# Kernel tuning notes

Hardware: AMD Instinct MI355X
Metric: run time of the kernel (lower is better)

## Reference

```python
import jax, jax.numpy as jnp
import numpy as np

B, T, V, S = 64, 512, 1296, 32
BLANK = 0
NEG = jnp.float32(-1e30)  # log-space -inf surrogate (keeps grads finite)


def setup_inputs() -> dict:
    key = jax.random.key(0)
    k1, k2 = jax.random.split(key)
    logits = jax.random.normal(k1, (B, T, V), dtype=jnp.float32)
    # CTC targets must not contain the blank index (0)
    targets = jax.random.randint(k2, (B, S), 1, V).astype(jnp.int64)
    input_lengths = jnp.full((B,), T, dtype=jnp.int32)
    target_lengths = jnp.full((B,), S, dtype=jnp.int32)
    return {"logits": logits, "targets": targets,
            "input_lengths": input_lengths, "target_lengths": target_lengths}


def _ctc_loss(log_probs, targets, input_lengths, target_lengths):
    """CTC negative log-likelihood, reduction='mean' (per-sample / target_len, then batch mean)."""
    Bb, Tt, Vv = log_probs.shape
    Ss = targets.shape[1]
    L = 2 * Ss + 1  # extended label sequence: blank-interleaved

    ext = jnp.full((Bb, L), BLANK, dtype=targets.dtype).at[:, 1::2].set(targets)  # (B,L)
    # log-prob of each extended label at each time: (B,T,L)
    lp_ext = jnp.take_along_axis(log_probs, jnp.broadcast_to(ext[:, None, :], (Bb, Tt, L)), axis=2)

    # transition s-2 -> s allowed iff ext[s] is non-blank (s odd) and ext[s] != ext[s-2]
    pos = jnp.arange(L)
    ext_m2 = jnp.pad(ext, ((0, 0), (2, 0)), constant_values=-1)[:, :L]
    skip_ok = (pos[None, :] % 2 == 1) & (ext != ext_m2)  # (B,L)

    alpha0 = (jnp.full((Bb, L), NEG)
              .at[:, 0].set(lp_ext[:, 0, 0])
              .at[:, 1].set(lp_ext[:, 0, 1]))

    def step(alpha, lp_t):
        a1 = alpha
        a2 = jnp.pad(alpha[:, :-1], ((0, 0), (1, 0)), constant_values=NEG)
        a3 = jnp.where(skip_ok, jnp.pad(alpha[:, :-2], ((0, 0), (2, 0)), constant_values=NEG), NEG)
        new = jnp.logaddexp(jnp.logaddexp(a1, a2), a3) + lp_t
        return new, new

    _, alphas_rest = jax.lax.scan(step, alpha0, jnp.swapaxes(lp_ext, 0, 1)[1:])  # (T-1,B,L)
    alphas = jnp.concatenate([alpha0[None], alphas_rest], axis=0)  # (T,B,L)

    bi = jnp.arange(Bb)
    alpha_last = alphas[input_lengths - 1, bi]  # (B,L)
    l_end = alpha_last[bi, 2 * target_lengths]       # final blank
    l_lab = alpha_last[bi, 2 * target_lengths - 1]   # final label
    nll = -jnp.logaddexp(l_end, l_lab)               # (B,)
    nll = jnp.where(jnp.isinf(nll) | (nll > 1e29), 0.0, nll)  # zero_infinity=True
    return jnp.mean(nll / target_lengths.astype(nll.dtype))    # reduction='mean'


def reference(logits, targets, input_lengths, target_lengths):
    log_probs = jax.nn.log_softmax(logits, axis=-1)
    return _ctc_loss(log_probs, targets, input_lengths, target_lengths)
```

## Files before the change

kernel.cpp:

```cpp
#include <hip/hip_runtime.h>
#include <math.h>

#define BB 64
#define TT 512
#define VV 1296
#define SS 32
#define NST 64
#define NG  (TT/4)
#define NEGV (-1e30f)
#define LOG2E 1.44269504088896340736f
#define LN2   0.69314718055994530942f

#define EXP2(x) __builtin_amdgcn_exp2f(x)
#define LOG2(x) __builtin_amdgcn_logf(x)

__device__ __forceinline__ float dpp_shr1(float old, float src) {
    return __int_as_float(__builtin_amdgcn_update_dpp(
        __float_as_int(old), __float_as_int(src), 0x138, 0xf, 0xf, false));
}
__device__ __forceinline__ float dpp_shl1(float old, float src) {
    return __int_as_float(__builtin_amdgcn_update_dpp(
        __float_as_int(old), __float_as_int(src), 0x130, 0xf, 0xf, false));
}

__global__ __launch_bounds__(256) void k_lse_gather(
    const float* __restrict__ logits,
    const int* __restrict__ targets,
    float* __restrict__ lp_ext,
    float* __restrict__ out)
{
    const int wid  = threadIdx.x >> 6;
    const int lane = threadIdx.x & 63;
    const int bt   = blockIdx.x * 4 + wid;
    const int b    = bt >> 9;
    const int t    = bt & (TT - 1);

    if (bt == 0 && lane == 0) out[0] = 0.f;

    const float* row = logits + (size_t)bt * VV;
    const float4* row4 = (const float4*)row;

    float4 v[5];
    #pragma unroll
    for (int k = 0; k < 5; ++k) v[k] = row4[lane + 64 * k];
    float4 vx = row4[320 + (lane & 3)];
    if (lane >= 4) { vx.x = NEGV; vx.y = NEGV; vx.z = NEGV; vx.w = NEGV; }

    float s = 0.f;
    #pragma unroll
    for (int k = 0; k < 5; ++k)
        s += __expf(v[k].x) + __expf(v[k].y) + __expf(v[k].z) + __expf(v[k].w);
    s += __expf(vx.x) + __expf(vx.y) + __expf(vx.z) + __expf(vx.w);
    #pragma unroll
    for (int off = 1; off < 64; off <<= 1) s += __shfl_xor(s, off, 64);

    const float norm = __logf(s);

    const int lab = (lane & 1) ? 0 : targets[b * SS + (lane >> 1)];
    const float lp2 = (row[lab] - norm) * LOG2E;
    lp_ext[(((size_t)b * NG + (t >> 2)) * NST + lane) * 4 + (t & 3)] = lp2;
}

#define PFV 6

__global__ __launch_bounds__(64) void k_alpha(
    const float* __restrict__ lp_ext,
    const int* __restrict__ targets,
    const int* __restrict__ in_len,
    const int* __restrict__ tgt_len,
    float* __restrict__ out)
{
    const int b    = blockIdx.x;
    const int lane = threadIdx.x;
    const float4* lpv = (const float4*)(lp_ext + (size_t)b * NG * NST * 4);
    const int Ti = in_len[b];
    const int Sb = tgt_len[b];

    bool skip = false;
    if (!(lane & 1) && lane >= 2) {
        const int j = lane >> 1;
        skip = (targets[b * SS + j] != targets[b * SS + j - 1]);
    }

    const float4 g0 = lpv[lane];

    float alpha = (lane == 0) ? g0.x : NEGV;
    float c0    = __shfl(g0.x, 1, 64);

#define STEP(LPS)                                                            \
    {                                                                        \
        const float lps_ = (LPS);                                            \
           \
        const float lpbk_ = (lane & 1) ? lps_ : dpp_shl1(lps_, lps_);        \
        const float a1_ = alpha;                                             \
        const float a2_ = dpp_shr1(c0, alpha);         \
        float a3_       = dpp_shr1(NEGV, a2_);               \
        a3_ = skip ? a3_ : NEGV;          \
        c0 += lpbk_;                                     \
        const float mx_ = fmaxf(fmaxf(a1_, a2_), a3_);           \
        const float ml_ = mx_ + lps_;                 \
        alpha = LOG2(EXP2(a1_ - mx_) + EXP2(a2_ - mx_) +                     \
                     EXP2(a3_ - mx_)) + ml_;                                 \
    }

    if (Ti > 1) STEP(g0.y);
    if (Ti > 2) STEP(g0.z);
    if (Ti > 3) STEP(g0.w);

    float4 bufv[PFV];
    #pragma unroll
    for (int i = 0; i < PFV; ++i) {
        int gg = 1 + i; if (gg > NG - 1) gg = NG - 1;
        bufv[i] = lpv[gg * NST + lane];
    }

    int g = 1;
    while (g + PFV <= NG) {
        #pragma unroll
        for (int i = 0; i < PFV; ++i) {
            const float4 cur = bufv[i];
            int gp = g + i + PFV; if (gp > NG - 1) gp = NG - 1;
            bufv[i] = lpv[(size_t)gp * NST + lane];
            const int t0 = (g + i) * 4;
            if (t0 + 3 < Ti) {
                STEP(cur.x); STEP(cur.y); STEP(cur.z); STEP(cur.w);
            } else {
                if (t0 + 0 < Ti) STEP(cur.x);
                if (t0 + 1 < Ti) STEP(cur.y);
                if (t0 + 2 < Ti) STEP(cur.z);
                if (t0 + 3 < Ti) STEP(cur.w);
            }
        }
        g += PFV;
    }
    #pragma unroll
    for (int i = 0; i < PFV; ++i) {
        const int gi = g + i;
        if (gi <= NG - 1) {
            const float4 cur = bufv[i];
            const int t0 = gi * 4;
            if (t0 + 3 < Ti) {
                STEP(cur.x); STEP(cur.y); STEP(cur.z); STEP(cur.w);
            } else {
                if (t0 + 0 < Ti) STEP(cur.x);
                if (t0 + 1 < Ti) STEP(cur.y);
                if (t0 + 2 < Ti) STEP(cur.z);
                if (t0 + 3 < Ti) STEP(cur.w);
            }
        }
    }
#undef STEP

    const float vll = __shfl(alpha, 2 * Sb - 2, 64);
    const float vle = __shfl(alpha, 2 * Sb - 1, 64);

    if (lane == 0) {
        const float mx = fmaxf(vle, vll);
        float nll = -LN2 * (mx + LOG2(EXP2(vle - mx) + EXP2(vll - mx)));
        if (isinf(nll) || nll > 1e29f) nll = 0.f;
        atomicAdd(out, nll / ((float)Sb * (float)BB));
    }
}

extern "C" void kernel_launch(void* const* d_in, const int* in_sizes, int n_in,
                              void* d_out, int out_size, void* d_ws, size_t ws_size,
                              hipStream_t stream) {
    const float* logits   = (const float*)d_in[0];
    const int*   targets  = (const int*)d_in[1];
    const int*   in_len   = (const int*)d_in[2];
    const int*   tgt_len  = (const int*)d_in[3];
    float*       out      = (float*)d_out;

    float* lp_ext = (float*)d_ws;

    k_lse_gather<<<BB * TT / 4, 256, 0, stream>>>(logits, targets, lp_ext, out);
    k_alpha<<<BB, 64, 0, stream>>>(lp_ext, targets, in_len, tgt_len, out);
}
```

Before: 270.7 us.

## Fuse log-softmax gather and alpha recursion via last-block-per-batch counter

Merges the two kernels into one launch. Each block computes log-softmax and gathers for 4 timesteps, then an atomic counter per batch lets the last finishing block run the sequential alpha recursion using coherent atomic loads. A second counter lets the final batch reduce the per-sample NLLs without a float atomicAdd. This removes a kernel launch boundary and lets alpha recursions for early-finishing batches overlap with remaining gather work. In exchange it adds a memset, atomic traffic and uncached coherent loads.

```diff
diff --git a/kernel.cpp b/kernel.cpp
--- a/kernel.cpp
+++ b/kernel.cpp
@@ -14,6 +14,8 @@
 #define EXP2(x) __builtin_amdgcn_exp2f(x)
 #define LOG2(x) __builtin_amdgcn_logf(x)
 
+#define PFV 6
+
 __device__ __forceinline__ float dpp_shr1(float old, float src) {
     return __int_as_float(__builtin_amdgcn_update_dpp(
         __float_as_int(old), __float_as_int(src), 0x138, 0xf, 0xf, false));
@@ -23,55 +25,74 @@
         __float_as_int(old), __float_as_int(src), 0x130, 0xf, 0xf, false));
 }
 
-__global__ __launch_bounds__(256) void k_lse_gather(
+__device__ __forceinline__ float4 load_f4_coherent(const float4* p) {
+    unsigned long long* q = (unsigned long long*)p;
+    unsigned long long lo = __hip_atomic_load(q,     __ATOMIC_RELAXED, __HIP_MEMORY_SCOPE_AGENT);
+    unsigned long long hi = __hip_atomic_load(q + 1, __ATOMIC_RELAXED, __HIP_MEMORY_SCOPE_AGENT);
+    float4 r;
+    r.x = __uint_as_float((unsigned int)lo);
+    r.y = __uint_as_float((unsigned int)(lo >> 32));
+    r.z = __uint_as_float((unsigned int)hi);
+    r.w = __uint_as_float((unsigned int)(hi >> 32));
+    return r;
+}
+
+__global__ __launch_bounds__(256) void k_ctc_fused(
     const float* __restrict__ logits,
     const int* __restrict__ targets,
+    const int* __restrict__ in_len,
+    const int* __restrict__ tgt_len,
+    unsigned int* __restrict__ cnt,
+    unsigned int* __restrict__ dcnt,
+    float* __restrict__ nlls,
     float* __restrict__ lp_ext,
     float* __restrict__ out)
 {
     const int wid  = threadIdx.x >> 6;
     const int lane = threadIdx.x & 63;
-    const int bt   = blockIdx.x * 4 + wid;
-    const int b    = bt >> 9;
-    const int t    = bt & (TT - 1);
-
-    if (bt == 0 && lane == 0) out[0] = 0.f;
-
-    const float* row = logits + (size_t)bt * VV;
-    const float4* row4 = (const float4*)row;
-
-    float4 v[5];
-    #pragma unroll
-    for (int k = 0; k < 5; ++k) v[k] = row4[lane + 64 * k];
-    float4 vx = row4[320 + (lane & 3)];
-    if (lane >= 4) { vx.x = NEGV; vx.y = NEGV; vx.z = NEGV; vx.w = NEGV; }
-
-    float s = 0.f;
-    #pragma unroll
-    for (int k = 0; k < 5; ++k)
-        s += __expf(v[k].x) + __expf(v[k].y) + __expf(v[k].z) + __expf(v[k].w);
-    s += __expf(vx.x) + __expf(vx.y) + __expf(vx.z) + __expf(vx.w);
-    #pragma unroll
-    for (int off = 1; off < 64; off <<= 1) s += __shfl_xor(s, off, 64);
-
-    const float norm = __logf(s);
-
-    const int lab = (lane & 1) ? 0 : targets[b * SS + (lane >> 1)];
-    const float lp2 = (row[lab] - norm) * LOG2E;
-    lp_ext[(((size_t)b * NG + (t >> 2)) * NST + lane) * 4 + (t & 3)] = lp2;
-}
-
-#define PFV 6
-
-__global__ __launch_bounds__(64) void k_alpha(
-    const float* __restrict__ lp_ext,
-    const int* __restrict__ targets,
-    const int* __restrict__ in_len,
-    const int* __restrict__ tgt_len,
-    float* __restrict__ out)
-{
-    const int b    = blockIdx.x;
-    const int lane = threadIdx.x;
+    const int b    = blockIdx.x >> 7;
+    const int g    = blockIdx.x & (NG - 1);
+    const int t    = g * 4 + wid;
+
+    {
+        const float* row = logits + (size_t)(b * TT + t) * VV;
+        const float4* row4 = (const float4*)row;
+
+        float4 v[5];
+        #pragma unroll
+        for (int k = 0; k < 5; ++k) v[k] = row4[lane + 64 * k];
+        float4 vx = row4[320 + (lane & 3)];
+        if (lane >= 4) { vx.x = NEGV; vx.y = NEGV; vx.z = NEGV; vx.w = NEGV; }
+
+        float s = 0.f;
+        #pragma unroll
+        for (int k = 0; k < 5; ++k)
+            s += __expf(v[k].x) + __expf(v[k].y) + __expf(v[k].z) + __expf(v[k].w);
+        s += __expf(vx.x) + __expf(vx.y) + __expf(vx.z) + __expf(vx.w);
+        #pragma unroll
+        for (int off = 1; off < 64; off <<= 1) s += __shfl_xor(s, off, 64);
+
+        const float norm = __logf(s);
+        const int lab = (lane & 1) ? 0 : targets[b * SS + (lane >> 1)];
+        const float lp2 = (row[lab] - norm) * LOG2E;
+
+        unsigned int* dst = (unsigned int*)
+            (lp_ext + ((((size_t)b * NG + g) * NST + lane) * 4 + wid));
+        __hip_atomic_store(dst, __float_as_uint(lp2),
+                           __ATOMIC_RELAXED, __HIP_MEMORY_SCOPE_AGENT);
+    }
+
+    __syncthreads();
+
+    if (wid != 0) return;
+
+    int old = -1;
+    if (lane == 0)
+        old = (int)__hip_atomic_fetch_add(&cnt[b], 1u,
+                                          __ATOMIC_ACQ_REL, __HIP_MEMORY_SCOPE_AGENT);
+    old = __shfl(old, 0, 64);
+    if (old != NG - 1) return;
+
     const float4* lpv = (const float4*)(lp_ext + (size_t)b * NG * NST * 4);
     const int Ti = in_len[b];
     const int Sb = tgt_len[b];
@@ -82,7 +103,7 @@
         skip = (targets[b * SS + j] != targets[b * SS + j - 1]);
     }
 
-    const float4 g0 = lpv[lane];
+    const float4 g0 = load_f4_coherent(&lpv[lane]);
 
     float alpha = (lane == 0) ? g0.x : NEGV;
     float c0    = __shfl(g0.x, 1, 64);
@@ -111,17 +132,17 @@
     #pragma unroll
     for (int i = 0; i < PFV; ++i) {
         int gg = 1 + i; if (gg > NG - 1) gg = NG - 1;
-        bufv[i] = lpv[gg * NST + lane];
-    }
-
-    int g = 1;
-    while (g + PFV <= NG) {
+        bufv[i] = load_f4_coherent(&lpv[gg * NST + lane]);
+    }
+
+    int gq = 1;
+    while (gq + PFV <= NG) {
         #pragma unroll
         for (int i = 0; i < PFV; ++i) {
             const float4 cur = bufv[i];
-            int gp = g + i + PFV; if (gp > NG - 1) gp = NG - 1;
-            bufv[i] = lpv[(size_t)gp * NST + lane];
-            const int t0 = (g + i) * 4;
+            int gp = gq + i + PFV; if (gp > NG - 1) gp = NG - 1;
+            bufv[i] = load_f4_coherent(&lpv[(size_t)gp * NST + lane]);
+            const int t0 = (gq + i) * 4;
             if (t0 + 3 < Ti) {
                 STEP(cur.x); STEP(cur.y); STEP(cur.z); STEP(cur.w);
             } else {
@@ -131,11 +152,11 @@
                 if (t0 + 3 < Ti) STEP(cur.w);
             }
         }
-        g += PFV;
+        gq += PFV;
     }
     #pragma unroll
     for (int i = 0; i < PFV; ++i) {
-        const int gi = g + i;
+        const int gi = gq + i;
         if (gi <= NG - 1) {
             const float4 cur = bufv[i];
             const int t0 = gi * 4;
@@ -154,12 +175,26 @@
     const float vll = __shfl(alpha, 2 * Sb - 2, 64);
     const float vle = __shfl(alpha, 2 * Sb - 1, 64);
 
+    int old2 = -1;
     if (lane == 0) {
         const float mx = fmaxf(vle, vll);
         float nll = -LN2 * (mx + LOG2(EXP2(vle - mx) + EXP2(vll - mx)));
         if (isinf(nll) || nll > 1e29f) nll = 0.f;
-        atomicAdd(out, nll / ((float)Sb * (float)BB));
-    }
+        __hip_atomic_store((unsigned int*)&nlls[b], __float_as_uint(nll / (float)Sb),
+                           __ATOMIC_RELAXED, __HIP_MEMORY_SCOPE_AGENT);
+        old2 = (int)__hip_atomic_fetch_add(dcnt, 1u,
+                                           __ATOMIC_ACQ_REL, __HIP_MEMORY_SCOPE_AGENT);
+    }
+    old2 = __shfl(old2, 0, 64);
+    if (old2 != BB - 1) return;
+
+    float vsum = __uint_as_float(__hip_atomic_load(
+        (unsigned int*)&nlls[lane], __ATOMIC_RELAXED, __HIP_MEMORY_SCOPE_AGENT));
+    #pragma unroll
+    for (int off = 1; off < 64; off <<= 1) vsum += __shfl_xor(vsum, off, 64);
+    if (lane == 0)
+        __hip_atomic_store((unsigned int*)out, __float_as_uint(vsum * (1.0f / (float)BB)),
+                           __ATOMIC_RELAXED, __HIP_MEMORY_SCOPE_AGENT);
 }
 
 extern "C" void kernel_launch(void* const* d_in, const int* in_sizes, int n_in,
@@ -171,8 +206,13 @@
     const int*   tgt_len  = (const int*)d_in[3];
     float*       out      = (float*)d_out;
 
-    float* lp_ext = (float*)d_ws;
-
-    k_lse_gather<<<BB * TT / 4, 256, 0, stream>>>(logits, targets, lp_ext, out);
-    k_alpha<<<BB, 64, 0, stream>>>(lp_ext, targets, in_len, tgt_len, out);
-}
+    unsigned int* cnt    = (unsigned int*)d_ws;
+    unsigned int* dcnt   = cnt + 64;
+    float*        nlls   = (float*)(cnt + 80);
+    float*        lp_ext = (float*)((char*)d_ws + 1024);
+
+    hipMemsetAsync(d_ws, 0, 512, stream);
+
+    k_ctc_fused<<<BB * NG, 256, 0, stream>>>(
+        logits, targets, in_len, tgt_len, cnt, dcnt, nlls, lp_ext, out);
+}
```

Result: slower. 689.9 us (+154.9%).
